# Kernel optimization log

Measured on AMD Instinct MI355X. Metric: run time of the kernel, lower is better.

The kernel has to match this reference:

```python
import jax, jax.numpy as jnp
import numpy as np
from jax import lax

N_ADAPTERS = 4
TOP_K = 2
TEMPERATURE = 1.0
ADAPTER_START = 2  # [base, static, adapter_0..3]


def setup_inputs() -> dict:
    key = jax.random.key(0)
    ks = jax.random.split(key, 10)
    B, S, D, H, RH = 4, 2048, 4096, 128, 64
    return {
        "h": jax.random.normal(ks[0], (B, S, D), jnp.float32),
        "static_delta": jax.random.normal(ks[1], (B, S, D), jnp.float32),
        "adapter_residuals": jax.random.normal(ks[2], (N_ADAPTERS, B, S, D), jnp.float32),
        "conflict_scores": jax.random.uniform(ks[3], (B, S, N_ADAPTERS), jnp.float32),
        "rel_proj_w": jax.random.normal(ks[4], (D, RH), jnp.float32) * 0.02,
        "rel_proj_b": jnp.zeros((RH,), jnp.float32),
        "rel_heads_w": jax.random.normal(ks[5], (RH, N_ADAPTERS), jnp.float32) * 0.02,
        "rel_heads_b": jnp.zeros((N_ADAPTERS,), jnp.float32),
        "gate_w1": jax.random.normal(ks[6], (D + 2 * N_ADAPTERS, H), jnp.float32) * 0.02,
        "gate_b1": jnp.zeros((H,), jnp.float32),
        "gate_w2": jax.random.normal(ks[7], (H, 2 + N_ADAPTERS), jnp.float32) * 0.02,
        "gate_b2": jnp.zeros((2 + N_ADAPTERS,), jnp.float32),
    }


def reference(h, static_delta, adapter_residuals, conflict_scores,
              rel_proj_w, rel_proj_b, rel_heads_w, rel_heads_b,
              gate_w1, gate_b1, gate_w2, gate_b2):
    # Reliability features: relu(Linear) -> per-adapter heads -> sigmoid, (B,S,A)
    feat = jax.nn.relu(jnp.einsum('bsd,dh->bsh', h, rel_proj_w) + rel_proj_b)
    rel = jax.nn.sigmoid(jnp.einsum('bsh,ha->bsa', feat, rel_heads_w) + rel_heads_b)

    # Gate MLP on [h, rel, conflict] -> (B,S,n_choices)
    gate_in = jnp.concatenate([h, rel, conflict_scores], axis=-1)
    hid = jax.nn.relu(jnp.einsum('bsf,fh->bsh', gate_in, gate_w1) + gate_b1)
    logits = (jnp.einsum('bsh,hc->bsc', hid, gate_w2) + gate_b2) / TEMPERATURE

    # Top-k mask over adapter logits (top_k < n_adapters)
    adapter_logits = logits[..., ADAPTER_START:]
    _, topk_idx = lax.top_k(adapter_logits, TOP_K)  # (B,S,K)
    keep = jax.nn.one_hot(topk_idx, N_ADAPTERS, dtype=bool).any(axis=-2)  # (B,S,A)
    masked = jnp.where(keep, adapter_logits, -jnp.inf)
    logits = jnp.concatenate([logits[..., :ADAPTER_START], masked], axis=-1)

    gates = jax.nn.softmax(logits, axis=-1)  # (B,S,6)

    # Weighted residual composition
    result = gates[..., 1:2] * static_delta  # static gate
    result = result + jnp.einsum('bsn,nbsd->bsd', gates[..., ADAPTER_START:], adapter_residuals)
    return result
```

## Files before the change

### kernel.cpp

```cpp
#include <hip/hip_runtime.h>
#include <math.h>


constexpr int D      = 4096;
constexpr int RH     = 64;
constexpr int HG     = 128;
constexpr int NA     = 4;
constexpr int NOUT   = RH + HG;
constexpr int TOKENS = 4 * 2048;
constexpr int M_BLK  = 32;
constexpr int KC     = 64;
constexpr int NCHUNK = D / KC;

__global__ __launch_bounds__(256, 1) void gates_kernel(
    const float* __restrict__ h,
    const float* __restrict__ conflict,
    const float* __restrict__ rpw, const float* __restrict__ rpb,
    const float* __restrict__ rhw, const float* __restrict__ rhb,
    const float* __restrict__ gw1, const float* __restrict__ gb1,
    const float* __restrict__ gw2, const float* __restrict__ gb2,
    float* __restrict__ coef)
{
    __shared__ float smem[KC * M_BLK + KC * NOUT];
    float* hT = smem;
    float* wT = smem + KC * M_BLK;

    const int tid  = threadIdx.x;
    const int tok0 = blockIdx.x * M_BLK;
    const int tg   = tid & 7;
    const int og   = tid >> 3;

    float4 hreg[2];
    float4 wreg[12];

    auto load_chunk = [&](int kc) {
        const int k0 = kc * KC;
#pragma unroll
        for (int r = 0; r < 2; ++r) {
            int q = tid + 256 * r;
            int tok = q >> 4, kq = q & 15;
            hreg[r] = *reinterpret_cast<const float4*>(
                h + (size_t)(tok0 + tok) * D + k0 + kq * 4);
        }
#pragma unroll
        for (int r = 0; r < 12; ++r) {
            int q = tid + 256 * r;
            int f = q * 4;
            int k = f / NOUT;
            int c = f - k * NOUT;
            const float* src = (c < RH)
                ? (rpw + (size_t)(k0 + k) * RH + c)
                : (gw1 + (size_t)(k0 + k) * HG + (c - RH));
            wreg[r] = *reinterpret_cast<const float4*>(src);
        }
    };
    auto store_chunk = [&]() {
#pragma unroll
        for (int r = 0; r < 2; ++r) {
            int q = tid + 256 * r;
            int tok = q >> 4, kq = q & 15;
            float v[4] = {hreg[r].x, hreg[r].y, hreg[r].z, hreg[r].w};
#pragma unroll
            for (int j = 0; j < 4; ++j) {
                int row = kq * 4 + j;
                int col = (tok + 4 * (row & 7)) & 31;
                hT[row * M_BLK + col] = v[j];
            }
        }
#pragma unroll
        for (int r = 0; r < 12; ++r)
            *reinterpret_cast<float4*>(wT + (size_t)(tid + 256 * r) * 4) = wreg[r];
    };

    float acc[4][6];
#pragma unroll
    for (int i = 0; i < 4; ++i)
#pragma unroll
        for (int j = 0; j < 6; ++j) acc[i][j] = 0.f;

    load_chunk(0);
    for (int kc = 0; kc < NCHUNK; ++kc) {
        __syncthreads();
        store_chunk();
        if (kc + 1 < NCHUNK) load_chunk(kc + 1);
        __syncthreads();

#pragma unroll 2
        for (int k = 0; k < KC; ++k) {
            const float4 hv = *reinterpret_cast<const float4*>(
                &hT[k * M_BLK + ((tg * 4 + 4 * (k & 7)) & 31)]);
            const float* wr = wT + k * NOUT + og * 6;
            float2 w0 = *reinterpret_cast<const float2*>(wr + 0);
            float2 w1 = *reinterpret_cast<const float2*>(wr + 2);
            float2 w2 = *reinterpret_cast<const float2*>(wr + 4);
            const float hh[4] = {hv.x, hv.y, hv.z, hv.w};
            const float ww[6] = {w0.x, w0.y, w1.x, w1.y, w2.x, w2.y};
#pragma unroll
            for (int i = 0; i < 4; ++i)
#pragma unroll
                for (int j = 0; j < 6; ++j)
                    acc[i][j] = fmaf(hh[i], ww[j], acc[i][j]);
        }
    }
    __syncthreads();

    float (*ob)[NOUT + 1] = reinterpret_cast<float (*)[NOUT + 1]>(smem);
#pragma unroll
    for (int i = 0; i < 4; ++i)
#pragma unroll
        for (int j = 0; j < 6; ++j)
            ob[tg * 4 + i][og * 6 + j] = acc[i][j];
    __syncthreads();

    if (tid < M_BLK) {
        const int t  = tid;
        const int gt = tok0 + t;

        float ra[NA] = {0.f, 0.f, 0.f, 0.f};
        for (int j = 0; j < RH; ++j) {
            float f = ob[t][j] + rpb[j];
            f = f > 0.f ? f : 0.f;
#pragma unroll
            for (int a = 0; a < NA; ++a) ra[a] = fmaf(f, rhw[j * NA + a], ra[a]);
        }
        float rel[NA], cf[NA];
#pragma unroll
        for (int a = 0; a < NA; ++a) {
            rel[a] = 1.f / (1.f + expf(-(ra[a] + rhb[a])));
            cf[a]  = conflict[(size_t)gt * NA + a];
        }

        float lg[6] = {0.f, 0.f, 0.f, 0.f, 0.f, 0.f};
        for (int i = 0; i < HG; ++i) {
            float v = ob[t][RH + i] + gb1[i];
#pragma unroll
            for (int a = 0; a < NA; ++a)
                v = fmaf(rel[a], gw1[(size_t)(D + a) * HG + i], v);
#pragma unroll
            for (int a = 0; a < NA; ++a)
                v = fmaf(cf[a], gw1[(size_t)(D + NA + a) * HG + i], v);
            v = v > 0.f ? v : 0.f;
#pragma unroll
            for (int c = 0; c < 6; ++c) lg[c] = fmaf(v, gw2[i * 6 + c], lg[c]);
        }
#pragma unroll
        for (int c = 0; c < 6; ++c) lg[c] += gb2[c];

        int i1 = 0;
#pragma unroll
        for (int a = 1; a < NA; ++a) if (lg[2 + a] > lg[2 + i1]) i1 = a;
        int i2 = (i1 == 0) ? 1 : 0;
#pragma unroll
        for (int a = 0; a < NA; ++a)
            if (a != i1 && lg[2 + a] > lg[2 + i2]) i2 = a;

        float m  = fmaxf(fmaxf(lg[0], lg[1]), fmaxf(lg[2 + i1], lg[2 + i2]));
        float e0 = expf(lg[0] - m), e1 = expf(lg[1] - m);
        float ea = expf(lg[2 + i1] - m), eb = expf(lg[2 + i2] - m);
        float inv = 1.f / (e0 + e1 + ea + eb);

        float out5[5] = {e1 * inv, 0.f, 0.f, 0.f, 0.f};
        out5[1 + i1] = ea * inv;
        out5[1 + i2] = eb * inv;
        float* cp = coef + (size_t)gt * 8;
#pragma unroll
        for (int s = 0; s < 5; ++s) cp[s] = out5[s];
    }
}

__global__ __launch_bounds__(256) void combine_kernel(
    const float* __restrict__ sd,
    const float* __restrict__ ar,
    const float* __restrict__ coef,
    float* __restrict__ out)
{
    const size_t NT4 = (size_t)TOKENS * (D / 4);
    const size_t stride = (size_t)gridDim.x * blockDim.x;
    const float4* sd4  = reinterpret_cast<const float4*>(sd);
    const float4* ar4  = reinterpret_cast<const float4*>(ar);
    float4*       out4 = reinterpret_cast<float4*>(out);

    for (size_t v = (size_t)blockIdx.x * blockDim.x + threadIdx.x;
         v < NT4; v += stride) {
        const int tok = (int)(v >> 10);
        const float* cp = coef + (size_t)tok * 8;
        const float cs = cp[0];
        float4 s = sd4[v];
        float4 o;
        o.x = cs * s.x; o.y = cs * s.y; o.z = cs * s.z; o.w = cs * s.w;
#pragma unroll
        for (int n = 0; n < NA; ++n) {
            const float cn = cp[1 + n];
            if (cn != 0.f) {
                float4 r = ar4[(size_t)n * NT4 + v];
                o.x = fmaf(cn, r.x, o.x); o.y = fmaf(cn, r.y, o.y);
                o.z = fmaf(cn, r.z, o.z); o.w = fmaf(cn, r.w, o.w);
            }
        }
        out4[v] = o;
    }
}

extern "C" void kernel_launch(void* const* d_in, const int* in_sizes, int n_in,
                              void* d_out, int out_size, void* d_ws, size_t ws_size,
                              hipStream_t stream) {
    const float* h   = (const float*)d_in[0];
    const float* sd  = (const float*)d_in[1];
    const float* ar  = (const float*)d_in[2];
    const float* cs  = (const float*)d_in[3];
    const float* rpw = (const float*)d_in[4];
    const float* rpb = (const float*)d_in[5];
    const float* rhw = (const float*)d_in[6];
    const float* rhb = (const float*)d_in[7];
    const float* gw1 = (const float*)d_in[8];
    const float* gb1 = (const float*)d_in[9];
    const float* gw2 = (const float*)d_in[10];
    const float* gb2 = (const float*)d_in[11];

    float* coef = (float*)d_ws;
    float* out  = (float*)d_out;

    hipLaunchKernelGGL(gates_kernel, dim3(TOKENS / M_BLK), dim3(256), 0, stream,
                       h, cs, rpw, rpb, rhw, rhb, gw1, gb1, gw2, gb2, coef);
    hipLaunchKernelGGL(combine_kernel, dim3(2048), dim3(256), 0, stream,
                       sd, ar, coef, out);
}
```

Baseline: 1.280 ms.

## Split gate GEMM over K into slices with separate reduction epilogue kernel

The fused gate kernel is split in two. The first kernel computes partial projections over four K-slices per token block, with a smaller chunk size and higher occupancy, and writes the partials into the output buffer as scratch. A second kernel sums the partials and runs the reliability, gate MLP, top-k and softmax epilogue for 64 tokens per block. This raises block count and occupancy on the GEMM-like stage, which before had only 256 blocks at one per CU. The cost is an extra launch and extra partial-sum traffic.

```diff
diff --git a/kernel.cpp b/kernel.cpp
--- a/kernel.cpp
+++ b/kernel.cpp
@@ -9,41 +9,41 @@
 constexpr int NOUT   = RH + HG;
 constexpr int TOKENS = 4 * 2048;
 constexpr int M_BLK  = 32;
-constexpr int KC     = 64;
-constexpr int NCHUNK = D / KC;
-
-__global__ __launch_bounds__(256, 1) void gates_kernel(
+constexpr int NSLICE = 4;
+constexpr int KSL    = D / NSLICE;
+constexpr int KC     = 32;
+constexpr int NCH    = KSL / KC;
+
+__global__ __launch_bounds__(256, 4) void gates_partial(
     const float* __restrict__ h,
-    const float* __restrict__ conflict,
-    const float* __restrict__ rpw, const float* __restrict__ rpb,
-    const float* __restrict__ rhw, const float* __restrict__ rhb,
-    const float* __restrict__ gw1, const float* __restrict__ gb1,
-    const float* __restrict__ gw2, const float* __restrict__ gb2,
-    float* __restrict__ coef)
+    const float* __restrict__ rpw,
+    const float* __restrict__ gw1,
+    float* __restrict__ part)
 {
     __shared__ float smem[KC * M_BLK + KC * NOUT];
     float* hT = smem;
     float* wT = smem + KC * M_BLK;
 
-    const int tid  = threadIdx.x;
-    const int tok0 = blockIdx.x * M_BLK;
-    const int tg   = tid & 7;
-    const int og   = tid >> 3;
-
-    float4 hreg[2];
-    float4 wreg[12];
+    const int tid   = threadIdx.x;
+    const int bt    = blockIdx.x >> 2;
+    const int sl    = blockIdx.x & 3;
+    const int tok0  = bt * M_BLK;
+    const int kbase = sl * KSL;
+    const int tg    = tid & 7;
+    const int og    = tid >> 3;
+
+    float4 hreg;
+    float4 wreg[6];
 
     auto load_chunk = [&](int kc) {
-        const int k0 = kc * KC;
-#pragma unroll
-        for (int r = 0; r < 2; ++r) {
-            int q = tid + 256 * r;
-            int tok = q >> 4, kq = q & 15;
-            hreg[r] = *reinterpret_cast<const float4*>(
+        const int k0 = kbase + kc * KC;
+        {
+            int tok = tid >> 3, kq = tid & 7;
+            hreg = *reinterpret_cast<const float4*>(
                 h + (size_t)(tok0 + tok) * D + k0 + kq * 4);
         }
 #pragma unroll
-        for (int r = 0; r < 12; ++r) {
+        for (int r = 0; r < 6; ++r) {
             int q = tid + 256 * r;
             int f = q * 4;
             int k = f / NOUT;
@@ -55,11 +55,9 @@
         }
     };
     auto store_chunk = [&]() {
-#pragma unroll
-        for (int r = 0; r < 2; ++r) {
-            int q = tid + 256 * r;
-            int tok = q >> 4, kq = q & 15;
-            float v[4] = {hreg[r].x, hreg[r].y, hreg[r].z, hreg[r].w};
+        {
+            int tok = tid >> 3, kq = tid & 7;
+            float v[4] = {hreg.x, hreg.y, hreg.z, hreg.w};
 #pragma unroll
             for (int j = 0; j < 4; ++j) {
                 int row = kq * 4 + j;
@@ -68,7 +66,7 @@
             }
         }
 #pragma unroll
-        for (int r = 0; r < 12; ++r)
+        for (int r = 0; r < 6; ++r)
             *reinterpret_cast<float4*>(wT + (size_t)(tid + 256 * r) * 4) = wreg[r];
     };
 
@@ -79,12 +77,11 @@
         for (int j = 0; j < 6; ++j) acc[i][j] = 0.f;
 
     load_chunk(0);
-    for (int kc = 0; kc < NCHUNK; ++kc) {
+    for (int kc = 0; kc < NCH; ++kc) {
         __syncthreads();
         store_chunk();
-        if (kc + 1 < NCHUNK) load_chunk(kc + 1);
+        if (kc + 1 < NCH) load_chunk(kc + 1);
         __syncthreads();
-
 #pragma unroll 2
         for (int k = 0; k < KC; ++k) {
             const float4 hv = *reinterpret_cast<const float4*>(
@@ -112,7 +109,49 @@
             ob[tg * 4 + i][og * 6 + j] = acc[i][j];
     __syncthreads();
 
-    if (tid < M_BLK) {
+    const size_t base = ((size_t)sl * TOKENS + tok0) * NOUT;
+#pragma unroll
+    for (int r = 0; r < 6; ++r) {
+        int q = tid + 256 * r;
+        int t = q / 48;
+        int c = (q - t * 48) * 4;
+        float4 v = {ob[t][c], ob[t][c + 1], ob[t][c + 2], ob[t][c + 3]};
+        *reinterpret_cast<float4*>(part + base + (size_t)t * NOUT + c) = v;
+    }
+}
+
+constexpr int TB2 = 64;
+
+__global__ __launch_bounds__(256) void gates_epilogue(
+    const float* __restrict__ part,
+    const float* __restrict__ conflict,
+    const float* __restrict__ rpb, const float* __restrict__ rhw,
+    const float* __restrict__ rhb, const float* __restrict__ gw1,
+    const float* __restrict__ gb1, const float* __restrict__ gw2,
+    const float* __restrict__ gb2,
+    float* __restrict__ coef)
+{
+    __shared__ float ob[TB2][NOUT + 1];
+    const int tid  = threadIdx.x;
+    const int tok0 = blockIdx.x * TB2;
+
+#pragma unroll
+    for (int r = 0; r < 12; ++r) {
+        int q = tid + 256 * r;
+        int t = q / 48;
+        int c = (q - t * 48) * 4;
+        float4 s = {0.f, 0.f, 0.f, 0.f};
+#pragma unroll
+        for (int sl = 0; sl < NSLICE; ++sl) {
+            const float4 v = *reinterpret_cast<const float4*>(
+                part + ((size_t)sl * TOKENS + tok0 + t) * NOUT + c);
+            s.x += v.x; s.y += v.y; s.z += v.z; s.w += v.w;
+        }
+        ob[t][c] = s.x; ob[t][c + 1] = s.y; ob[t][c + 2] = s.z; ob[t][c + 3] = s.w;
+    }
+    __syncthreads();
+
+    if (tid < TB2) {
         const int t  = tid;
         const int gt = tok0 + t;
 
@@ -217,11 +256,14 @@
     const float* gw2 = (const float*)d_in[10];
     const float* gb2 = (const float*)d_in[11];
 
+    float* part = (float*)d_out;
     float* coef = (float*)d_ws;
     float* out  = (float*)d_out;
 
-    hipLaunchKernelGGL(gates_kernel, dim3(TOKENS / M_BLK), dim3(256), 0, stream,
-                       h, cs, rpw, rpb, rhw, rhb, gw1, gb1, gw2, gb2, coef);
+    hipLaunchKernelGGL(gates_partial, dim3(256 * NSLICE), dim3(256), 0, stream,
+                       h, rpw, gw1, part);
+    hipLaunchKernelGGL(gates_epilogue, dim3(TOKENS / TB2), dim3(256), 0, stream,
+                       part, cs, rpb, rhw, rhb, gw1, gb1, gw2, gb2, coef);
     hipLaunchKernelGGL(combine_kernel, dim3(2048), dim3(256), 0, stream,
                        sd, ar, coef, out);
 }
```

After: 1.195 ms. -6.7%, faster.
